# Kernel optimization log

Measured on AMD Instinct MI355X. Metric: run time of the kernel, lower is better.

## Reference

```python
import jax, jax.numpy as jnp
import numpy as np

N = 100000
F_IN = 128
HID = 256
NUM_CLASSES = 64
E = 1600000


def setup_inputs() -> dict:
    key = jax.random.key(0)
    ks = jax.random.split(key, 10)
    x = jax.random.normal(ks[0], (N, F_IN), dtype=jnp.float32)
    edge_index = jax.random.randint(ks[1], (2, E), 0, N, dtype=jnp.int32)
    edge_weight = jax.random.uniform(ks[2], (E,), dtype=jnp.float32)
    def glorot(k, shape):
        lim = np.sqrt(6.0 / (shape[0] + shape[1]))
        return jax.random.uniform(k, shape, jnp.float32, -lim, lim)
    W0 = glorot(ks[3], (F_IN, HID)); b0 = jnp.zeros((HID,), jnp.float32)
    W1 = glorot(ks[4], (HID, HID)); b1 = jnp.zeros((HID,), jnp.float32)
    W2 = glorot(ks[5], (HID, NUM_CLASSES)); b2 = jnp.zeros((NUM_CLASSES,), jnp.float32)
    return {"x": x, "edge_index": edge_index, "edge_weight": edge_weight,
            "W0": W0, "b0": b0, "W1": W1, "b1": b1, "W2": W2, "b2": b2}


def _gcn_norm(edge_index, edge_weight, n_nodes):
    # renormalization trick: add self-loops (weight 1), D^-1/2 A D^-1/2
    loop = jnp.arange(n_nodes, dtype=edge_index.dtype)
    src = jnp.concatenate([edge_index[0], loop])
    dst = jnp.concatenate([edge_index[1], loop])
    w = jnp.concatenate([edge_weight, jnp.ones((n_nodes,), edge_weight.dtype)])
    deg = jax.ops.segment_sum(w, dst, num_segments=n_nodes)
    d_inv_sqrt = jnp.where(deg > 0, jax.lax.rsqrt(jnp.maximum(deg, 1e-12)), 0.0)
    norm = d_inv_sqrt[src] * w * d_inv_sqrt[dst]
    return src, dst, norm


def _gcn_layer(x, src, dst, norm, W, b, act):
    h = x @ W                                  # [N, d_out] project first (cheap dense)
    msg = h[src] * norm[:, None]               # [E+N, d_out] gather + scale
    out = jax.ops.segment_sum(msg, dst, num_segments=x.shape[0]) + b
    return act(out) if act is not None else out


def reference(x, edge_index, edge_weight, W0, b0, W1, b1, W2, b2):
    n_nodes = x.shape[0]
    src, dst, norm = _gcn_norm(edge_index, edge_weight, n_nodes)
    # dropout is identity at inference (training=None)
    h = _gcn_layer(x, src, dst, norm, W0, b0, jax.nn.relu)
    h = _gcn_layer(h, src, dst, norm, W1, b1, jax.nn.relu)
    h = _gcn_layer(h, src, dst, norm, W2, b2, None)
    return h
```

## Files before the change

kernel.cpp:

```cpp
#include <hip/hip_runtime.h>

#define N_NODES 100000
#define F_IN 128
#define HID 256
#define NCLS 64
#define N_EDGES 1600000

typedef _Float16 f16;
typedef f16 half8 __attribute__((ext_vector_type(8)));
typedef f16 half4 __attribute__((ext_vector_type(4)));
typedef float f32x4 __attribute__((ext_vector_type(4)));

#define FIXED_SCALE 67108864.0f

__global__ void k_init(unsigned long long* __restrict__ degp, int n) {
    int i = blockIdx.x * 256 + threadIdx.x;
    if (i < n) degp[i] = (unsigned long long)(1u << 26);
}

__global__ void k_deg(const int* __restrict__ dst, const float* __restrict__ w,
                      unsigned long long* __restrict__ degp, int e) {
    int i = blockIdx.x * 256 + threadIdx.x;
    if (i < e) {
        unsigned long long c = (1ULL << 40) |
            (unsigned long long)__float2uint_rn(w[i] * FIXED_SCALE);
        atomicAdd(&degp[dst[i]], c);
    }
}

__global__ void k_dis(const unsigned long long* __restrict__ degp,
                      float* __restrict__ dis, float* __restrict__ selfnorm,
                      int* __restrict__ cnt, int n) {
    int i = blockIdx.x * 256 + threadIdx.x;
    if (i < n) {
        unsigned long long p = degp[i];
        int c = (int)(p >> 40);
        float deg = (float)(p & ((1ULL << 40) - 1)) * (1.0f / FIXED_SCALE);
        float d = rsqrtf(deg);
        dis[i] = d;
        selfnorm[i] = d * d;
        cnt[i] = c;
    }
}

__global__ void k_scan1(const int* __restrict__ cnt, int* __restrict__ incl,
                        int* __restrict__ bsum, int n) {
    __shared__ int s[256];
    int t = threadIdx.x;
    int i = blockIdx.x * 256 + t;
    int v = (i < n) ? cnt[i] : 0;
    s[t] = v;
    __syncthreads();
    #pragma unroll
    for (int off = 1; off < 256; off <<= 1) {
        int x = (t >= off) ? s[t - off] : 0;
        __syncthreads();
        s[t] += x;
        __syncthreads();
    }
    if (i < n) incl[i] = s[t];
    if (t == 255) bsum[blockIdx.x] = s[255];
}

__global__ void k_scan2(const int* __restrict__ bsum, int* __restrict__ boff, int nb) {
    __shared__ int s[512];
    int t = threadIdx.x;
    int v = (t < nb) ? bsum[t] : 0;
    s[t] = v;
    __syncthreads();
    #pragma unroll
    for (int off = 1; off < 512; off <<= 1) {
        int x = (t >= off) ? s[t - off] : 0;
        __syncthreads();
        s[t] += x;
        __syncthreads();
    }
    if (t < nb) boff[t] = s[t] - v;
}

__global__ void k_scan3(int* __restrict__ row, const int* __restrict__ cnt,
                        const int* __restrict__ boff, int n) {
    int i = blockIdx.x * 256 + threadIdx.x;
    if (i < n) row[i] = row[i] - cnt[i] + boff[i >> 8];
}

__global__ void k_scatter(const int* __restrict__ src, const int* __restrict__ dst,
                          const float* __restrict__ w, const float* __restrict__ dis,
                          int* __restrict__ row, int2* __restrict__ csr, int e) {
    int i = blockIdx.x * 256 + threadIdx.x;
    if (i < e) {
        int s = src[i], d = dst[i];
        float nw = dis[s] * w[i] * dis[d];
        int pos = atomicAdd(&row[d], 1);
        csr[pos] = make_int2(s, __float_as_int(nw));
    }
}

__global__ void k_f32_to_f16(const float* __restrict__ src, f16* __restrict__ dst, int n4) {
    int i = blockIdx.x * 256 + threadIdx.x;
    if (i < n4) {
        float4 v = *(const float4*)&src[(size_t)i * 4];
        half4 o;
        o[0] = (f16)v.x; o[1] = (f16)v.y; o[2] = (f16)v.z; o[3] = (f16)v.w;
        *(half4*)&dst[(size_t)i * 4] = o;
    }
}

__global__ void k_wt(const float* __restrict__ W, f16* __restrict__ Wt, int K, int D) {
    int i = blockIdx.x * 256 + threadIdx.x;
    if (i < K * D) {
        int k = i / D, d = i % D;
        Wt[d * K + k] = (f16)W[i];
    }
}

template <int K, int DOUT, bool BIAS_RELU>
__global__ __launch_bounds__(256) void gemm_mfma(const f16* __restrict__ in,
                                                 const f16* __restrict__ Wt,
                                                 const float* __restrict__ bias,
                                                 f16* __restrict__ out,
                                                 int nNodes) {
    constexpr int BM = 128, BN = 64, BK = 32;
    constexpr int AP = 40;
    constexpr int CP = 72;
    constexpr int SMEM = (BM * AP + BN * AP) > (BM * CP) ? (BM * AP + BN * AP) : (BM * CP);
    __shared__ f16 smem[SMEM];
    f16* As = smem;
    f16* Bs = smem + BM * AP;

    const int t = threadIdx.x;
    const int w = t >> 6;
    const int lane = t & 63;
    const int quad = lane >> 4;
    const int l16 = lane & 15;
    const int nodeBase = blockIdx.x * BM;
    const int colBase = blockIdx.y * BN;

    f32x4 acc[2][4] = {};

    for (int k0 = 0; k0 < K; k0 += BK) {
        {
            int koff = (t & 3) * 8;
            #pragma unroll
            for (int p = 0; p < 2; ++p) {
                int r = (t >> 2) + p * 64;
                int gn = nodeBase + r;
                if (gn >= nNodes) gn = nNodes - 1;
                half8 v = *(const half8*)&in[(size_t)gn * K + k0 + koff];
                *(half8*)&As[r * AP + koff] = v;
            }
        }
        {
            int koff = (t & 3) * 8;
            int c = t >> 2;
            half8 v = *(const half8*)&Wt[(size_t)(colBase + c) * K + k0 + koff];
            *(half8*)&Bs[c * AP + koff] = v;
        }
        __syncthreads();

        half8 a[2];
        #pragma unroll
        for (int rt = 0; rt < 2; ++rt)
            a[rt] = *(const half8*)&As[(w * 32 + rt * 16 + l16) * AP + quad * 8];
        #pragma unroll
        for (int ct = 0; ct < 4; ++ct) {
            half8 b = *(const half8*)&Bs[(ct * 16 + l16) * AP + quad * 8];
            acc[0][ct] = __builtin_amdgcn_mfma_f32_16x16x32_f16(a[0], b, acc[0][ct], 0, 0, 0);
            acc[1][ct] = __builtin_amdgcn_mfma_f32_16x16x32_f16(a[1], b, acc[1][ct], 0, 0, 0);
        }
        __syncthreads();
    }

    float bv[4];
    #pragma unroll
    for (int ct = 0; ct < 4; ++ct)
        bv[ct] = BIAS_RELU ? bias[colBase + ct * 16 + l16] : 0.0f;

    f16* Cs = smem;
    #pragma unroll
    for (int rt = 0; rt < 2; ++rt)
        #pragma unroll
        for (int ct = 0; ct < 4; ++ct)
            #pragma unroll
            for (int r = 0; r < 4; ++r) {
                int rr = w * 32 + rt * 16 + quad * 4 + r;
                int cc = ct * 16 + l16;
                float v = acc[rt][ct][r];
                if (BIAS_RELU) v = fmaxf(v + bv[ct], 0.0f);
                Cs[rr * CP + cc] = (f16)v;
            }
    __syncthreads();
    #pragma unroll
    for (int p = 0; p < 4; ++p) {
        int r = (t >> 3) + p * 32;
        int gn = nodeBase + r;
        int chunk = (t & 7) * 8;
        if (gn < nNodes)
            *(half8*)&out[(size_t)gn * DOUT + colBase + chunk] =
                *(const half8*)&Cs[r * CP + chunk];
    }
}

template <int DOUT, int TPN, bool HAS_BIAS, bool OUT_F32>
__global__ __launch_bounds__(256) void agg_csr(const f16* __restrict__ h,
                                               const int2* __restrict__ csr,
                                               const int* __restrict__ row,
                                               const int* __restrict__ cnt,
                                               const float* __restrict__ sn,
                                               const float* __restrict__ bias,
                                               void* __restrict__ outv, int nNodes) {
    constexpr int NPB = 256 / TPN;
    int node = blockIdx.x * NPB + threadIdx.x / TPN;
    if (node >= nNodes) return;
    int lane = threadIdx.x % TPN;
    int col = lane * 8;

    float s = sn[node];
    half8 hv = *(const half8*)&h[(size_t)node * DOUT + col];
    float acc[8];
    #pragma unroll
    for (int i = 0; i < 8; ++i)
        acc[i] = s * (float)hv[i] + (HAS_BIAS ? bias[col + i] : 0.0f);

    int end = row[node];
    int e = end - cnt[node];
    for (; e + 1 < end; e += 2) {
        int2 e0 = csr[e], e1 = csr[e + 1];
        float w0 = __int_as_float(e0.y), w1 = __int_as_float(e1.y);
        half8 a0 = *(const half8*)&h[(size_t)e0.x * DOUT + col];
        half8 a1 = *(const half8*)&h[(size_t)e1.x * DOUT + col];
        #pragma unroll
        for (int i = 0; i < 8; ++i) acc[i] += w0 * (float)a0[i] + w1 * (float)a1[i];
    }
    if (e < end) {
        int2 e0 = csr[e];
        float w0 = __int_as_float(e0.y);
        half8 a0 = *(const half8*)&h[(size_t)e0.x * DOUT + col];
        #pragma unroll
        for (int i = 0; i < 8; ++i) acc[i] += w0 * (float)a0[i];
    }

    if (OUT_F32) {
        float* out = (float*)outv;
        float4 r0 = make_float4(acc[0], acc[1], acc[2], acc[3]);
        float4 r1 = make_float4(acc[4], acc[5], acc[6], acc[7]);
        *(float4*)&out[(size_t)node * DOUT + col] = r0;
        *(float4*)&out[(size_t)node * DOUT + col + 4] = r1;
    } else {
        f16* out = (f16*)outv;
        half8 o;
        #pragma unroll
        for (int i = 0; i < 8; ++i) o[i] = (f16)acc[i];
        *(half8*)&out[(size_t)node * DOUT + col] = o;
    }
}

extern "C" void kernel_launch(void* const* d_in, const int* in_sizes, int n_in,
                              void* d_out, int out_size, void* d_ws, size_t ws_size,
                              hipStream_t stream) {
    const float* x  = (const float*)d_in[0];
    const int*   ei = (const int*)d_in[1];
    const float* ew = (const float*)d_in[2];
    const float* W0 = (const float*)d_in[3];
    const float* b0 = (const float*)d_in[4];
    const float* W1 = (const float*)d_in[5];
    const float* b1 = (const float*)d_in[6];
    const float* W2 = (const float*)d_in[7];
    const float* b2 = (const float*)d_in[8];
    const int* src = ei;
    const int* dst = ei + N_EDGES;
    float* outp = (float*)d_out;

    char* ws = (char*)d_ws;
    unsigned long long* degp = (unsigned long long*)ws;  ws += N_NODES * 8;
    float* dis      = (float*)ws;  ws += N_NODES * 4;
    float* selfnorm = (float*)ws;  ws += N_NODES * 4;
    int*   cnt      = (int*)ws;    ws += N_NODES * 4;
    int*   row      = (int*)ws;    ws += N_NODES * 4;
    int*   bsum     = (int*)ws;    ws += 512 * 4;
    int*   boff     = (int*)ws;    ws += 512 * 4;
    int2*  csr      = (int2*)ws;   ws += (size_t)N_EDGES * 8;
    f16*   xh       = (f16*)ws;    ws += (size_t)N_NODES * F_IN * 2;
    f16*   Wt0      = (f16*)ws;    ws += F_IN * HID * 2;
    f16*   Wt1      = (f16*)ws;    ws += HID * HID * 2;
    f16*   Wt2      = (f16*)ws;    ws += HID * NCLS * 2;
    f16*   bufA     = (f16*)ws;    ws += (size_t)N_NODES * HID * 2;
    f16*   bufB     = (f16*)ws;    ws += (size_t)N_NODES * HID * 2;

    const int nb = (N_NODES + 255) / 256;
    const int eb = (N_EDGES + 255) / 256;

    k_init<<<nb, 256, 0, stream>>>(degp, N_NODES);
    k_deg<<<eb, 256, 0, stream>>>(dst, ew, degp, N_EDGES);
    k_dis<<<nb, 256, 0, stream>>>(degp, dis, selfnorm, cnt, N_NODES);
    k_scan1<<<nb, 256, 0, stream>>>(cnt, row, bsum, N_NODES);
    k_scan2<<<1, 512, 0, stream>>>(bsum, boff, nb);
    k_scan3<<<nb, 256, 0, stream>>>(row, cnt, boff, N_NODES);
    k_scatter<<<eb, 256, 0, stream>>>(src, dst, ew, dis, row, csr, N_EDGES);

    k_f32_to_f16<<<(N_NODES * (F_IN / 4) + 255) / 256, 256, 0, stream>>>(x, xh, N_NODES * (F_IN / 4));
    k_wt<<<(F_IN * HID + 255) / 256, 256, 0, stream>>>(W0, Wt0, F_IN, HID);
    k_wt<<<(HID * HID + 255) / 256, 256, 0, stream>>>(W1, Wt1, HID, HID);
    k_wt<<<(HID * NCLS + 255) / 256, 256, 0, stream>>>(W2, Wt2, HID, NCLS);

    const int gX = (N_NODES + 127) / 128;

    agg_csr<F_IN, 16, false, false><<<(N_NODES + 15) / 16, 256, 0, stream>>>(
        xh, csr, row, cnt, selfnorm, nullptr, bufA, N_NODES);
    gemm_mfma<F_IN, HID, true><<<dim3(gX, HID / 64), 256, 0, stream>>>(bufA, Wt0, b0, bufB, N_NODES);

    agg_csr<HID, 32, false, false><<<(N_NODES + 7) / 8, 256, 0, stream>>>(
        bufB, csr, row, cnt, selfnorm, nullptr, bufA, N_NODES);
    gemm_mfma<HID, HID, true><<<dim3(gX, HID / 64), 256, 0, stream>>>(bufA, Wt1, b1, bufB, N_NODES);

    gemm_mfma<HID, NCLS, false><<<dim3(gX, NCLS / 64), 256, 0, stream>>>(bufB, Wt2, nullptr, bufA, N_NODES);
    agg_csr<NCLS, 8, true, true><<<(N_NODES + 31) / 32, 256, 0, stream>>>(
        bufA, csr, row, cnt, selfnorm, b2, outp, N_NODES);
}
```

Before: 598.7 us.

## Rework degree computation via CSR, enlarge GEMM tile with register prefetch, unroll aggregation

Degree normalization no longer uses 64-bit packed fixed-point atomics. It now counts edges with int atomics, scatters raw weights into the CSR, then sums degrees per segment and rescales the CSR weights in two extra passes. The MFMA GEMM tile grows from 128 to 256 rows and prefetches the next K-slice into registers before the MFMAs run. The aggregation loop is unrolled from two to four edges. These changes aim to reduce atomic cost and raise memory-level parallelism, at the price of extra CSR passes, higher register pressure and fewer GEMM blocks.

```diff
diff --git a/kernel.cpp b/kernel.cpp
--- a/kernel.cpp
+++ b/kernel.cpp
@@ -11,36 +11,14 @@
 typedef f16 half4 __attribute__((ext_vector_type(4)));
 typedef float f32x4 __attribute__((ext_vector_type(4)));
 
-#define FIXED_SCALE 67108864.0f
-
-__global__ void k_init(unsigned long long* __restrict__ degp, int n) {
-    int i = blockIdx.x * 256 + threadIdx.x;
-    if (i < n) degp[i] = (unsigned long long)(1u << 26);
-}
-
-__global__ void k_deg(const int* __restrict__ dst, const float* __restrict__ w,
-                      unsigned long long* __restrict__ degp, int e) {
-    int i = blockIdx.x * 256 + threadIdx.x;
-    if (i < e) {
-        unsigned long long c = (1ULL << 40) |
-            (unsigned long long)__float2uint_rn(w[i] * FIXED_SCALE);
-        atomicAdd(&degp[dst[i]], c);
-    }
-}
-
-__global__ void k_dis(const unsigned long long* __restrict__ degp,
-                      float* __restrict__ dis, float* __restrict__ selfnorm,
-                      int* __restrict__ cnt, int n) {
-    int i = blockIdx.x * 256 + threadIdx.x;
-    if (i < n) {
-        unsigned long long p = degp[i];
-        int c = (int)(p >> 40);
-        float deg = (float)(p & ((1ULL << 40) - 1)) * (1.0f / FIXED_SCALE);
-        float d = rsqrtf(deg);
-        dis[i] = d;
-        selfnorm[i] = d * d;
-        cnt[i] = c;
-    }
+__global__ void k_zero(int* __restrict__ cnt, int n) {
+    int i = blockIdx.x * 256 + threadIdx.x;
+    if (i < n) cnt[i] = 0;
+}
+
+__global__ void k_cnt(const int* __restrict__ dst, int* __restrict__ cnt, int e) {
+    int i = blockIdx.x * 256 + threadIdx.x;
+    if (i < e) atomicAdd(&cnt[dst[i]], 1);
 }
 
 __global__ void k_scan1(const int* __restrict__ cnt, int* __restrict__ incl,
@@ -85,14 +63,44 @@
 }
 
 __global__ void k_scatter(const int* __restrict__ src, const int* __restrict__ dst,
-                          const float* __restrict__ w, const float* __restrict__ dis,
+                          const float* __restrict__ w,
                           int* __restrict__ row, int2* __restrict__ csr, int e) {
     int i = blockIdx.x * 256 + threadIdx.x;
     if (i < e) {
-        int s = src[i], d = dst[i];
-        float nw = dis[s] * w[i] * dis[d];
+        int d = dst[i];
         int pos = atomicAdd(&row[d], 1);
-        csr[pos] = make_int2(s, __float_as_int(nw));
+        csr[pos] = make_int2(src[i], __float_as_int(w[i]));
+    }
+}
+
+__global__ void k_segdeg(const int2* __restrict__ csr, const int* __restrict__ row,
+                         const int* __restrict__ cnt, float* __restrict__ dis,
+                         float* __restrict__ selfnorm, int n) {
+    int i = blockIdx.x * 256 + threadIdx.x;
+    if (i >= n) return;
+    int end = row[i];
+    int st = end - cnt[i];
+    float s = 1.0f;
+    for (int e = st; e < end; ++e) s += __int_as_float(csr[e].y);
+    float d = rsqrtf(s);
+    dis[i] = d;
+    selfnorm[i] = d * d;
+}
+
+__global__ void k_renorm(int2* __restrict__ csr, const int* __restrict__ row,
+                         const int* __restrict__ cnt, const float* __restrict__ dis,
+                         int n) {
+    int g = blockIdx.x * 256 + threadIdx.x;
+    int node = g >> 2;
+    if (node >= n) return;
+    int lane = g & 3;
+    int end = row[node];
+    int st = end - cnt[node];
+    float dd = dis[node];
+    for (int e = st + lane; e < end; e += 4) {
+        int2 v = csr[e];
+        float nw = dis[v.x] * __int_as_float(v.y) * dd;
+        csr[e].y = __float_as_int(nw);
     }
 }
 
@@ -120,13 +128,15 @@
                                                  const float* __restrict__ bias,
                                                  f16* __restrict__ out,
                                                  int nNodes) {
-    constexpr int BM = 128, BN = 64, BK = 32;
+    constexpr int BM = 256, BN = 64, BK = 32;
     constexpr int AP = 40;
     constexpr int CP = 72;
-    constexpr int SMEM = (BM * AP + BN * AP) > (BM * CP) ? (BM * AP + BN * AP) : (BM * CP);
+    constexpr int SA = BM * AP;
+    constexpr int SB = BN * AP;
+    constexpr int SMEM = (SA + SB) > (BM * CP) ? (SA + SB) : (BM * CP);
     __shared__ f16 smem[SMEM];
     f16* As = smem;
-    f16* Bs = smem + BM * AP;
+    f16* Bs = smem + SA;
 
     const int t = threadIdx.x;
     const int w = t >> 6;
@@ -136,38 +146,50 @@
     const int nodeBase = blockIdx.x * BM;
     const int colBase = blockIdx.y * BN;
 
-    f32x4 acc[2][4] = {};
+    const int ar = t >> 2;
+    const int ak = (t & 3) * 8;
+
+    half8 aReg[4];
+    half8 bReg;
+    #pragma unroll
+    for (int p = 0; p < 4; ++p) {
+        int gn = nodeBase + ar + p * 64;
+        if (gn >= nNodes) gn = nNodes - 1;
+        aReg[p] = *(const half8*)&in[(size_t)gn * K + ak];
+    }
+    bReg = *(const half8*)&Wt[(size_t)(colBase + ar) * K + ak];
+
+    f32x4 acc[4][4] = {};
 
     for (int k0 = 0; k0 < K; k0 += BK) {
-        {
-            int koff = (t & 3) * 8;
+        #pragma unroll
+        for (int p = 0; p < 4; ++p)
+            *(half8*)&As[(ar + p * 64) * AP + ak] = aReg[p];
+        *(half8*)&Bs[ar * AP + ak] = bReg;
+        __syncthreads();
+
+        if (k0 + BK < K) {
             #pragma unroll
-            for (int p = 0; p < 2; ++p) {
-                int r = (t >> 2) + p * 64;
-                int gn = nodeBase + r;
+            for (int p = 0; p < 4; ++p) {
+                int gn = nodeBase + ar + p * 64;
                 if (gn >= nNodes) gn = nNodes - 1;
-                half8 v = *(const half8*)&in[(size_t)gn * K + k0 + koff];
-                *(half8*)&As[r * AP + koff] = v;
+                aReg[p] = *(const half8*)&in[(size_t)gn * K + k0 + BK + ak];
             }
+            bReg = *(const half8*)&Wt[(size_t)(colBase + ar) * K + k0 + BK + ak];
         }
-        {
-            int koff = (t & 3) * 8;
-            int c = t >> 2;
-            half8 v = *(const half8*)&Wt[(size_t)(colBase + c) * K + k0 + koff];
-            *(half8*)&Bs[c * AP + koff] = v;
-        }
-        __syncthreads();
-
-        half8 a[2];
-        #pragma unroll
-        for (int rt = 0; rt < 2; ++rt)
-            a[rt] = *(const half8*)&As[(w * 32 + rt * 16 + l16) * AP + quad * 8];
-        #pragma unroll
-        for (int ct = 0; ct < 4; ++ct) {
-            half8 b = *(const half8*)&Bs[(ct * 16 + l16) * AP + quad * 8];
-            acc[0][ct] = __builtin_amdgcn_mfma_f32_16x16x32_f16(a[0], b, acc[0][ct], 0, 0, 0);
-            acc[1][ct] = __builtin_amdgcn_mfma_f32_16x16x32_f16(a[1], b, acc[1][ct], 0, 0, 0);
-        }
+
+        half8 a[4], b[4];
+        #pragma unroll
+        for (int rt = 0; rt < 4; ++rt)
+            a[rt] = *(const half8*)&As[(w * 64 + rt * 16 + l16) * AP + quad * 8];
+        #pragma unroll
+        for (int ct = 0; ct < 4; ++ct)
+            b[ct] = *(const half8*)&Bs[(ct * 16 + l16) * AP + quad * 8];
+        #pragma unroll
+        for (int rt = 0; rt < 4; ++rt)
+            #pragma unroll
+            for (int ct = 0; ct < 4; ++ct)
+                acc[rt][ct] = __builtin_amdgcn_mfma_f32_16x16x32_f16(a[rt], b[ct], acc[rt][ct], 0, 0, 0);
         __syncthreads();
     }
 
@@ -178,20 +200,19 @@
 
     f16* Cs = smem;
     #pragma unroll
-    for (int rt = 0; rt < 2; ++rt)
+    for (int rt = 0; rt < 4; ++rt)
         #pragma unroll
         for (int ct = 0; ct < 4; ++ct)
             #pragma unroll
             for (int r = 0; r < 4; ++r) {
-                int rr = w * 32 + rt * 16 + quad * 4 + r;
-                int cc = ct * 16 + l16;
+                int rr = w * 64 + rt * 16 + quad * 4 + r;
                 float v = acc[rt][ct][r];
                 if (BIAS_RELU) v = fmaxf(v + bv[ct], 0.0f);
-                Cs[rr * CP + cc] = (f16)v;
+                Cs[rr * CP + ct * 16 + l16] = (f16)v;
             }
     __syncthreads();
     #pragma unroll
-    for (int p = 0; p < 4; ++p) {
+    for (int p = 0; p < 8; ++p) {
         int r = (t >> 3) + p * 32;
         int gn = nodeBase + r;
         int chunk = (t & 7) * 8;
@@ -224,15 +245,20 @@
 
     int end = row[node];
     int e = end - cnt[node];
-    for (; e + 1 < end; e += 2) {
-        int2 e0 = csr[e], e1 = csr[e + 1];
+    for (; e + 3 < end; e += 4) {
+        int2 e0 = csr[e], e1 = csr[e + 1], e2 = csr[e + 2], e3 = csr[e + 3];
         float w0 = __int_as_float(e0.y), w1 = __int_as_float(e1.y);
+        float w2 = __int_as_float(e2.y), w3 = __int_as_float(e3.y);
         half8 a0 = *(const half8*)&h[(size_t)e0.x * DOUT + col];
         half8 a1 = *(const half8*)&h[(size_t)e1.x * DOUT + col];
-        #pragma unroll
-        for (int i = 0; i < 8; ++i) acc[i] += w0 * (float)a0[i] + w1 * (float)a1[i];
-    }
-    if (e < end) {
+        half8 a2 = *(const half8*)&h[(size_t)e2.x * DOUT + col];
+        half8 a3 = *(const half8*)&h[(size_t)e3.x * DOUT + col];
+        #pragma unroll
+        for (int i = 0; i < 8; ++i)
+            acc[i] += w0 * (float)a0[i] + w1 * (float)a1[i] +
+                      w2 * (float)a2[i] + w3 * (float)a3[i];
+    }
+    for (; e < end; ++e) {
         int2 e0 = csr[e];
         float w0 = __int_as_float(e0.y);
         half8 a0 = *(const half8*)&h[(size_t)e0.x * DOUT + col];
@@ -272,14 +298,13 @@
     float* outp = (float*)d_out;
 
     char* ws = (char*)d_ws;
-    unsigned long long* degp = (unsigned long long*)ws;  ws += N_NODES * 8;
+    int2*  csr      = (int2*)ws;   ws += (size_t)N_EDGES * 8;
     float* dis      = (float*)ws;  ws += N_NODES * 4;
     float* selfnorm = (float*)ws;  ws += N_NODES * 4;
     int*   cnt      = (int*)ws;    ws += N_NODES * 4;
     int*   row      = (int*)ws;    ws += N_NODES * 4;
     int*   bsum     = (int*)ws;    ws += 512 * 4;
     int*   boff     = (int*)ws;    ws += 512 * 4;
-    int2*  csr      = (int2*)ws;   ws += (size_t)N_EDGES * 8;
     f16*   xh       = (f16*)ws;    ws += (size_t)N_NODES * F_IN * 2;
     f16*   Wt0      = (f16*)ws;    ws += F_IN * HID * 2;
     f16*   Wt1      = (f16*)ws;    ws += HID * HID * 2;
@@ -290,20 +315,21 @@
     const int nb = (N_NODES + 255) / 256;
     const int eb = (N_EDGES + 255) / 256;
 
-    k_init<<<nb, 256, 0, stream>>>(degp, N_NODES);
-    k_deg<<<eb, 256, 0, stream>>>(dst, ew, degp, N_EDGES);
-    k_dis<<<nb, 256, 0, stream>>>(degp, dis, selfnorm, cnt, N_NODES);
+    k_zero<<<nb, 256, 0, stream>>>(cnt, N_NODES);
+    k_cnt<<<eb, 256, 0, stream>>>(dst, cnt, N_EDGES);
     k_scan1<<<nb, 256, 0, stream>>>(cnt, row, bsum, N_NODES);
     k_scan2<<<1, 512, 0, stream>>>(bsum, boff, nb);
     k_scan3<<<nb, 256, 0, stream>>>(row, cnt, boff, N_NODES);
-    k_scatter<<<eb, 256, 0, stream>>>(src, dst, ew, dis, row, csr, N_EDGES);
+    k_scatter<<<eb, 256, 0, stream>>>(src, dst, ew, row, csr, N_EDGES);
+    k_segdeg<<<nb, 256, 0, stream>>>(csr, row, cnt, dis, selfnorm, N_NODES);
+    k_renorm<<<(N_NODES * 4 + 255) / 256, 256, 0, stream>>>(csr, row, cnt, dis, N_NODES);
 
     k_f32_to_f16<<<(N_NODES * (F_IN / 4) + 255) / 256, 256, 0, stream>>>(x, xh, N_NODES * (F_IN / 4));
     k_wt<<<(F_IN * HID + 255) / 256, 256, 0, stream>>>(W0, Wt0, F_IN, HID);
     k_wt<<<(HID * HID + 255) / 256, 256, 0, stream>>>(W1, Wt1, HID, HID);
     k_wt<<<(HID * NCLS + 255) / 256, 256, 0, stream>>>(W2, Wt2, HID, NCLS);
 
-    const int gX = (N_NODES + 127) / 128;
+    const int gX = (N_NODES + 255) / 256;
 
     agg_csr<F_IN, 16, false, false><<<(N_NODES + 15) / 16, 256, 0, stream>>>(
         xh, csr, row, cnt, selfnorm, nullptr, bufA, N_NODES);
```

New measurement: 644.2 us. +7.6%, slower.
